# Performance work log

Measured on AMD Instinct MI355X. Metric: run time of the kernel, lower is better.

The kernel has to match this reference:

```python
import jax, jax.numpy as jnp
import numpy as np

N = 50000       # nodes
E = 600000      # edges (before self-loops)
D_IN, D_H, D_OUT, D_E = 128, 128, 64, 8
NEG_SLOPE = 0.2


def _glorot(key, shape):
    fan = shape[0]
    return jax.random.normal(key, shape, dtype=jnp.float32) / jnp.sqrt(jnp.float32(fan))


def setup_inputs() -> dict:
    key = jax.random.key(0)
    ks = iter(jax.random.split(key, 32))
    inp = {
        "x": jax.random.normal(next(ks), (N, D_IN), dtype=jnp.float32),
        "edge_index": jax.random.randint(next(ks), (2, E), 0, N, dtype=jnp.int64),
        "edge_attr": jax.random.normal(next(ks), (E, D_E), dtype=jnp.float32),
    }
    dims = [(D_IN, D_H), (D_H, D_H), (D_H, D_OUT)]  # 3 GATConv layers, heads=1
    for i, (din, dout) in enumerate(dims):
        inp[f"W{i}"] = _glorot(next(ks), (din, dout))
        inp[f"as{i}"] = _glorot(next(ks), (dout,))
        inp[f"ad{i}"] = _glorot(next(ks), (dout,))
        inp[f"We{i}"] = _glorot(next(ks), (D_E, dout))
        inp[f"ae{i}"] = _glorot(next(ks), (dout,))
        inp[f"b{i}"] = jnp.zeros((dout,), dtype=jnp.float32)
    return inp


def _add_self_loops(src, dst, edge_attr, n):
    # PyG add_self_loops(fill_value='mean'): self-loop attr = mean of incoming edge attrs
    deg = jax.ops.segment_sum(jnp.ones_like(dst, dtype=edge_attr.dtype), dst, num_segments=n)
    mean_attr = jax.ops.segment_sum(edge_attr, dst, num_segments=n) / jnp.maximum(deg, 1.0)[:, None]
    loop = jnp.arange(n, dtype=src.dtype)
    return (jnp.concatenate([src, loop]),
            jnp.concatenate([dst, loop]),
            jnp.concatenate([edge_attr, mean_attr], axis=0))


def _gat_layer(x, src, dst, edge_attr, W, a_s, a_d, We, a_e, b, n):
    h = x @ W                                   # [N, C] linear projection
    alpha = (h @ a_s)[src] + (h @ a_d)[dst] + (edge_attr @ We) @ a_e   # [Etot]
    alpha = jax.nn.leaky_relu(alpha, NEG_SLOPE)
    m = jax.ops.segment_max(alpha, dst, num_segments=n)                # segment softmax over dst
    ex = jnp.exp(alpha - m[dst])
    denom = jax.ops.segment_sum(ex, dst, num_segments=n)
    w = ex / (denom[dst] + 1e-16)
    return jax.ops.segment_sum(h[src] * w[:, None], dst, num_segments=n) + b


def reference(x, edge_index, edge_attr,
              W0, as0, ad0, We0, ae0, b0,
              W1, as1, ad1, We1, ae1, b1,
              W2, as2, ad2, We2, ae2, b2):
    n = x.shape[0]
    src, dst, ea = _add_self_loops(edge_index[0], edge_index[1], edge_attr, n)
    h = jax.nn.relu(_gat_layer(x, src, dst, ea, W0, as0, ad0, We0, ae0, b0, n))
    h = jax.nn.relu(_gat_layer(h, src, dst, ea, W1, as1, ad1, We1, ae1, b1, n))
    return _gat_layer(h, src, dst, ea, W2, as2, ad2, We2, ae2, b2, n)
```

## Files before the change

### kernel.cpp

```cpp
#include <hip/hip_runtime.h>
#include <hip/hip_fp16.h>
#include <cstdint>

#define NEG_SLOPE 0.2f
#define LOG2E 1.4426950408889634f
#define MAXD 64

typedef _Float16 f16;
typedef __attribute__((ext_vector_type(8))) _Float16 f16x8;
typedef __attribute__((ext_vector_type(4))) float f32x4;


__global__ void k_zero(int* __restrict__ p, int n) {
    int i = blockIdx.x * blockDim.x + threadIdx.x;
    if (i < n) p[i] = 0;
}

__global__ void k_wt(const float* __restrict__ W0, const float* __restrict__ W1,
                     const float* __restrict__ W2, f16* __restrict__ Wt0,
                     f16* __restrict__ Wt1, f16* __restrict__ Wt2) {
    int i = blockIdx.x * 256 + threadIdx.x;
    if (i < 16384) {
        int k = i >> 7, c = i & 127;
        Wt0[c * 128 + k] = (f16)W0[i];
    } else if (i < 32768) {
        int j = i - 16384; int k = j >> 7, c = j & 127;
        Wt1[c * 128 + k] = (f16)W1[j];
    } else if (i < 40960) {
        int j = i - 32768; int k = j >> 6, c = j & 63;
        Wt2[c * 128 + k] = (f16)W2[j];
    }
}

__global__ void k_count_fill(const int* __restrict__ src, const int* __restrict__ dst,
                             const float* __restrict__ ea,
                             const float* __restrict__ We0, const float* __restrict__ ae0,
                             const float* __restrict__ We1, const float* __restrict__ ae1,
                             const float* __restrict__ We2, const float* __restrict__ ae2,
                             int* __restrict__ deg, ushort4* __restrict__ ed, int E) {
    __shared__ float swea[24];
    int tid = threadIdx.x;
    if (tid < 24) {
        int layer = tid >> 3, k = tid & 7;
        const float* We = layer == 0 ? We0 : (layer == 1 ? We1 : We2);
        const float* ae = layer == 0 ? ae0 : (layer == 1 ? ae1 : ae2);
        int D = layer == 2 ? 64 : 128;
        float s = 0.f;
        for (int t = 0; t < D; t++) s = fmaf(We[(size_t)k * D + t], ae[t], s);
        swea[tid] = s;
    }
    __syncthreads();
    int e = blockIdx.x * blockDim.x + tid;
    if (e >= E) return;
    int s = src[e];
    int d = dst[e];
    int r = atomicAdd(deg + d, 1);
    if (r > MAXD - 1) r = MAXD - 1;
    float4 a0 = *(const float4*)&ea[(size_t)e * 8];
    float4 a1 = *(const float4*)&ea[(size_t)e * 8 + 4];
    float4 w00 = *(const float4*)&swea[0],  w01 = *(const float4*)&swea[4];
    float4 w10 = *(const float4*)&swea[8],  w11 = *(const float4*)&swea[12];
    float4 w20 = *(const float4*)&swea[16], w21 = *(const float4*)&swea[20];
    float d0 = a0.x*w00.x + a0.y*w00.y + a0.z*w00.z + a0.w*w00.w
             + a1.x*w01.x + a1.y*w01.y + a1.z*w01.z + a1.w*w01.w;
    float d1 = a0.x*w10.x + a0.y*w10.y + a0.z*w10.z + a0.w*w10.w
             + a1.x*w11.x + a1.y*w11.y + a1.z*w11.z + a1.w*w11.w;
    float d2 = a0.x*w20.x + a0.y*w20.y + a0.z*w20.z + a0.w*w20.w
             + a1.x*w21.x + a1.y*w21.y + a1.z*w21.z + a1.w*w21.w;
    ushort4 rec;
    rec.x = (unsigned short)s;
    rec.y = __half_as_ushort(__float2half(d0));
    rec.z = __half_as_ushort(__float2half(d1));
    rec.w = __half_as_ushort(__float2half(d2));
    ed[(size_t)d * MAXD + r] = rec;
}


template<int DOUT, bool XHALF>
__global__ __launch_bounds__(256) void k_gemm_mfma(
    const void* __restrict__ X_, const f16* __restrict__ Wt,
    const float* __restrict__ as_, const float* __restrict__ ad_,
    __half* __restrict__ H, float* __restrict__ hs, float* __restrict__ hd, int n)
{
    constexpr int NT = DOUT / 16;
    int lane = threadIdx.x & 63;
    int wave = threadIdx.x >> 6;
    int row0 = (blockIdx.x * 4 + wave) * 16;
    if (row0 >= n) return;
    int lrow = lane & 15;
    int kgrp = lane >> 4;
    int arow = row0 + lrow;
    bool aok = arow < n;

    f32x4 acc[NT] = {};

#pragma unroll
    for (int kt = 0; kt < 128; kt += 32) {
        f16x8 a = {};
        if (aok) {
            if constexpr (XHALF) {
                a = *(const f16x8*)((const f16*)X_ + (size_t)arow * 128 + kt + 8 * kgrp);
            } else {
                const float* xp = (const float*)X_ + (size_t)arow * 128 + kt + 8 * kgrp;
                float4 x0 = *(const float4*)xp;
                float4 x1 = *(const float4*)(xp + 4);
                f16x8 t = { (f16)x0.x, (f16)x0.y, (f16)x0.z, (f16)x0.w,
                            (f16)x1.x, (f16)x1.y, (f16)x1.z, (f16)x1.w };
                a = t;
            }
        }
#pragma unroll
        for (int nt = 0; nt < NT; nt++) {
            f16x8 b = *(const f16x8*)(Wt + (size_t)(nt * 16 + lrow) * 128 + kt + 8 * kgrp);
            acc[nt] = __builtin_amdgcn_mfma_f32_16x16x32_f16(a, b, acc[nt], 0, 0, 0);
        }
    }

    float asv[NT], adv[NT];
#pragma unroll
    for (int nt = 0; nt < NT; nt++) {
        asv[nt] = as_[nt * 16 + lrow];
        adv[nt] = ad_[nt * 16 + lrow];
    }

#pragma unroll
    for (int r = 0; r < 4; r++) {
        int row = row0 + 4 * kgrp + r;
        bool rok = row < n;
        float ps = 0.f, pd = 0.f;
#pragma unroll
        for (int nt = 0; nt < NT; nt++) {
            float v = acc[nt][r];
            ps = fmaf(v, asv[nt], ps);
            pd = fmaf(v, adv[nt], pd);
            if (rok) H[(size_t)row * DOUT + nt * 16 + lrow] = __float2half(v);
        }
#pragma unroll
        for (int off = 8; off; off >>= 1) {
            ps += __shfl_xor(ps, off);
            pd += __shfl_xor(pd, off);
        }
        if (rok && lrow == 0) { hs[row] = ps; hd[row] = pd; }
    }
}


template<int CPL>
__device__ __forceinline__ void accum_row16(float* acc, const __half* __restrict__ hrow,
                                            int l, float w) {
    if constexpr (CPL == 8) {
        float4 raw = *(const float4*)(hrow + 8 * l);
        __half2* h = (__half2*)&raw;
#pragma unroll
        for (int i = 0; i < 4; i++) {
            float2 f = __half22float2(h[i]);
            acc[2 * i]     = fmaf(w, f.x, acc[2 * i]);
            acc[2 * i + 1] = fmaf(w, f.y, acc[2 * i + 1]);
        }
    } else {
        float2 raw = *(const float2*)(hrow + 4 * l);
        __half2* h = (__half2*)&raw;
#pragma unroll
        for (int i = 0; i < 2; i++) {
            float2 f = __half22float2(h[i]);
            acc[2 * i]     = fmaf(w, f.x, acc[2 * i]);
            acc[2 * i + 1] = fmaf(w, f.y, acc[2 * i + 1]);
        }
    }
}

__device__ __forceinline__ float unpack_w(unsigned int p) {
    return __half2float(__ushort_as_half((unsigned short)(p & 0xFFFFu)));
}

__device__ __forceinline__ float fexp(float x) {
    return exp2f(x * LOG2E);
}

template<int DOUT, bool RELU, int LCOMP, bool OUT_HALF>
__global__ void k_aggregate(const __half* __restrict__ H,
                            const int* __restrict__ deg, const ushort4* __restrict__ edata,
                            const float* __restrict__ hs, const float* __restrict__ hd,
                            const float* __restrict__ bias, void* __restrict__ out_, int n) {
    int t = blockIdx.x * blockDim.x + threadIdx.x;
    int wid = t >> 6, lane = t & 63;
    if (wid >= n) return;
    int d = deg[wid]; if (d > MAXD) d = MAXD;
    int start = wid << 6;
    int quarter = lane >> 4, l = lane & 15;
    float hdv = hd[wid];
    float hsw = hs[wid];

    constexpr int CPL = DOUT / 16;
    float acc[CPL] = {};

    float al = -3.0e38f; int s = 0; float eadv = 0.f;
    if (lane < d) {
        ushort4 pv = edata[start + lane];
        s = pv.x;
        unsigned short eu = (LCOMP == 1) ? pv.y : (LCOMP == 2) ? pv.z : pv.w;
        eadv = __half2float(__ushort_as_half(eu));
        float a = hs[s] + hdv + eadv;
        al = a > 0.f ? a : NEG_SLOPE * a;
    }
    float esum = (lane < d) ? eadv : 0.f;
    float m0 = al;
#pragma unroll
    for (int off = 32; off; off >>= 1) {
        esum += __shfl_xor(esum, off);
        m0 = fmaxf(m0, __shfl_xor(m0, off));
    }
    int dd = d < 1 ? 1 : d;
    float aself = hsw + hdv + esum / (float)dd;
    aself = aself > 0.f ? aself : NEG_SLOPE * aself;
    float m = fmaxf(m0, aself);

    float ex = (lane < d) ? fexp(al - m) : 0.f;
    float exsum = ex;
#pragma unroll
    for (int off = 32; off; off >>= 1) exsum += __shfl_xor(exsum, off);
    float exself = fexp(aself - m);
    float denom = exsum + exself;

    unsigned int pk = ((unsigned int)s << 16) |
                      (unsigned int)__half_as_ushort(__float2half(ex));

    if (quarter == 0) accum_row16<CPL>(acc, H + (size_t)wid * DOUT, l, exself);

    int quads = (d + 3) >> 2;
#pragma unroll 4
    for (int jj = 0; jj < quads; jj++) {
        int j = 4 * jj + quarter;
        unsigned int pj = (unsigned int)__shfl((int)pk, j);
        int sj = pj >> 16;
        float w = unpack_w(pj);
        if (j < d) accum_row16<CPL>(acc, H + ((size_t)sj << (CPL == 8 ? 7 : 6)), l, w);
    }

#pragma unroll
    for (int v = 0; v < CPL; v++) {
        acc[v] += __shfl_xor(acc[v], 16);
        acc[v] += __shfl_xor(acc[v], 32);
    }

    if (lane < 16) {
        float inv = 1.0f / (denom + 1e-16f);
        float o[CPL];
#pragma unroll
        for (int v = 0; v < CPL; v++) {
            o[v] = acc[v] * inv + bias[CPL * l + v];
            if (RELU) o[v] = fmaxf(o[v], 0.f);
        }
        if constexpr (OUT_HALF) {
            __half* outh = (__half*)out_;
            __half2 p[CPL / 2];
#pragma unroll
            for (int v = 0; v < CPL / 2; v++) p[v] = __floats2half2_rn(o[2 * v], o[2 * v + 1]);
            if constexpr (CPL == 8) {
                *(uint4*)&outh[(size_t)wid * DOUT + 8 * l] = *(uint4*)p;
            } else {
                *(uint2*)&outh[(size_t)wid * DOUT + 4 * l] = *(uint2*)p;
            }
        } else {
            float* outf = (float*)out_;
            if constexpr (CPL == 8) {
                float4 o0 = { o[0], o[1], o[2], o[3] };
                float4 o1 = { o[4], o[5], o[6], o[7] };
                *(float4*)&outf[(size_t)wid * DOUT + 8 * l] = o0;
                *(float4*)&outf[(size_t)wid * DOUT + 8 * l + 4] = o1;
            } else {
                float4 ov = { o[0], o[1], o[2], o[3] };
                *(float4*)&outf[(size_t)wid * DOUT + 4 * l] = ov;
            }
        }
    }
}


extern "C" void kernel_launch(void* const* d_in, const int* in_sizes, int n_in,
                              void* d_out, int out_size, void* d_ws, size_t ws_size,
                              hipStream_t stream) {
    const float* x     = (const float*)d_in[0];
    const int*   eidx  = (const int*)d_in[1];
    const float* eattr = (const float*)d_in[2];
    const int N = in_sizes[0] / 128;
    const int E = in_sizes[1] / 2;
    const int* src = eidx;
    const int* dst = eidx + E;

    char* ws = (char*)d_ws;
    size_t off = 0;
    auto alloc = [&](size_t bytes) -> void* {
        void* p = ws + off;
        off += (bytes + 255) & ~(size_t)255;
        return p;
    };
    __half*  bufA = (__half*)alloc((size_t)N * 128 * sizeof(__half));
    __half*  hbuf = (__half*)alloc((size_t)N * 128 * sizeof(__half));
    int*     deg  = (int*)alloc((size_t)N * sizeof(int));
    float*   hs   = (float*)alloc((size_t)N * sizeof(float));
    float*   hd   = (float*)alloc((size_t)N * sizeof(float));
    ushort4* ed   = (ushort4*)alloc((size_t)N * MAXD * sizeof(ushort4));
    f16*     Wt0  = (f16*)alloc(16384 * sizeof(f16));
    f16*     Wt1  = (f16*)alloc(16384 * sizeof(f16));
    f16*     Wt2  = (f16*)alloc(8192 * sizeof(f16));

    const int tb = 256;

    k_zero<<<(N + tb - 1) / tb, tb, 0, stream>>>(deg, N);
    k_wt<<<160, 256, 0, stream>>>((const float*)d_in[3], (const float*)d_in[9],
                                  (const float*)d_in[15], Wt0, Wt1, Wt2);
    k_count_fill<<<(E + tb - 1) / tb, tb, 0, stream>>>(
        src, dst, eattr,
        (const float*)d_in[6], (const float*)d_in[7],
        (const float*)d_in[12], (const float*)d_in[13],
        (const float*)d_in[18], (const float*)d_in[19],
        deg, ed, E);

    int nwave_blocks = (N * 64 + tb - 1) / tb;
    int gemm_blocks = (N + 63) / 64;

    {
        const float* as_ = (const float*)d_in[4];
        const float* ad_ = (const float*)d_in[5];
        const float* b   = (const float*)d_in[8];
        k_gemm_mfma<128, false><<<gemm_blocks, 256, 0, stream>>>(x, Wt0, as_, ad_, hbuf, hs, hd, N);
        k_aggregate<128, true, 1, true><<<nwave_blocks, tb, 0, stream>>>(hbuf, deg, ed, hs, hd, b, bufA, N);
    }
    {
        const float* as_ = (const float*)d_in[10];
        const float* ad_ = (const float*)d_in[11];
        const float* b   = (const float*)d_in[14];
        k_gemm_mfma<128, true><<<gemm_blocks, 256, 0, stream>>>(bufA, Wt1, as_, ad_, hbuf, hs, hd, N);
        k_aggregate<128, true, 2, true><<<nwave_blocks, tb, 0, stream>>>(hbuf, deg, ed, hs, hd, b, bufA, N);
    }
    {
        const float* as_ = (const float*)d_in[16];
        const float* ad_ = (const float*)d_in[17];
        const float* b   = (const float*)d_in[20];
        k_gemm_mfma<64, true><<<gemm_blocks, 256, 0, stream>>>(bufA, Wt2, as_, ad_, hbuf, hs, hd, N);
        k_aggregate<64, false, 3, false><<<nwave_blocks, tb, 0, stream>>>(hbuf, deg, ed, hs, hd, b, d_out, N);
    }
}
```

Measured before the change: 226.8 us.

## Split edge count/fill, co-schedule fill with layer-0 GEMM, two nodes per wave

Edge degree counting moves into its own kernel that records per-edge rank, and the edge-attention precompute moves into the weight-transpose kernel. The edge fill then runs in the same launch as the layer-0 GEMM, with blocks interleaved so the two independent workloads overlap. Aggregation now handles two destination nodes per wave (32 lanes each), with a looped fallback for nodes of degree above 32, so fewer lanes sit idle at the average degree of about 12. This adds an extra kernel launch and a rank array round-trip through memory, and half-wave processing serialises more gather iterations per node.

```diff
diff --git a/kernel.cpp b/kernel.cpp
--- a/kernel.cpp
+++ b/kernel.cpp
@@ -16,9 +16,22 @@
     if (i < n) p[i] = 0;
 }
 
+__global__ void k_count(const int* __restrict__ dst, int* __restrict__ deg,
+                        unsigned short* __restrict__ rank, int E) {
+    int e = blockIdx.x * blockDim.x + threadIdx.x;
+    if (e < E) {
+        int r = atomicAdd(deg + dst[e], 1);
+        rank[e] = (unsigned short)(r > MAXD - 1 ? MAXD - 1 : r);
+    }
+}
+
 __global__ void k_wt(const float* __restrict__ W0, const float* __restrict__ W1,
                      const float* __restrict__ W2, f16* __restrict__ Wt0,
-                     f16* __restrict__ Wt1, f16* __restrict__ Wt2) {
+                     f16* __restrict__ Wt1, f16* __restrict__ Wt2,
+                     const float* __restrict__ We0, const float* __restrict__ ae0,
+                     const float* __restrict__ We1, const float* __restrict__ ae1,
+                     const float* __restrict__ We2, const float* __restrict__ ae2,
+                     float* __restrict__ wea) {
     int i = blockIdx.x * 256 + threadIdx.x;
     if (i < 16384) {
         int k = i >> 7, c = i & 127;
@@ -29,38 +42,34 @@
     } else if (i < 40960) {
         int j = i - 32768; int k = j >> 6, c = j & 63;
         Wt2[c * 128 + k] = (f16)W2[j];
-    }
-}
-
-__global__ void k_count_fill(const int* __restrict__ src, const int* __restrict__ dst,
-                             const float* __restrict__ ea,
-                             const float* __restrict__ We0, const float* __restrict__ ae0,
-                             const float* __restrict__ We1, const float* __restrict__ ae1,
-                             const float* __restrict__ We2, const float* __restrict__ ae2,
-                             int* __restrict__ deg, ushort4* __restrict__ ed, int E) {
-    __shared__ float swea[24];
-    int tid = threadIdx.x;
-    if (tid < 24) {
-        int layer = tid >> 3, k = tid & 7;
+    } else if (i < 40984) {
+        int j = i - 40960;
+        int layer = j >> 3, k = j & 7;
         const float* We = layer == 0 ? We0 : (layer == 1 ? We1 : We2);
         const float* ae = layer == 0 ? ae0 : (layer == 1 ? ae1 : ae2);
         int D = layer == 2 ? 64 : 128;
         float s = 0.f;
         for (int t = 0; t < D; t++) s = fmaf(We[(size_t)k * D + t], ae[t], s);
-        swea[tid] = s;
-    }
-    __syncthreads();
-    int e = blockIdx.x * blockDim.x + tid;
+        wea[j] = s;
+    }
+}
+
+
+__device__ __forceinline__ void fill_body(
+    int bid, int tid,
+    const int* __restrict__ src, const int* __restrict__ dst,
+    const unsigned short* __restrict__ rank, const float* __restrict__ ea,
+    const float* __restrict__ wea, ushort4* __restrict__ ed, int E)
+{
+    int e = bid * 256 + tid;
     if (e >= E) return;
     int s = src[e];
-    int d = dst[e];
-    int r = atomicAdd(deg + d, 1);
-    if (r > MAXD - 1) r = MAXD - 1;
+    int pos = dst[e] * MAXD + (int)rank[e];
     float4 a0 = *(const float4*)&ea[(size_t)e * 8];
     float4 a1 = *(const float4*)&ea[(size_t)e * 8 + 4];
-    float4 w00 = *(const float4*)&swea[0],  w01 = *(const float4*)&swea[4];
-    float4 w10 = *(const float4*)&swea[8],  w11 = *(const float4*)&swea[12];
-    float4 w20 = *(const float4*)&swea[16], w21 = *(const float4*)&swea[20];
+    float4 w00 = *(const float4*)&wea[0],  w01 = *(const float4*)&wea[4];
+    float4 w10 = *(const float4*)&wea[8],  w11 = *(const float4*)&wea[12];
+    float4 w20 = *(const float4*)&wea[16], w21 = *(const float4*)&wea[20];
     float d0 = a0.x*w00.x + a0.y*w00.y + a0.z*w00.z + a0.w*w00.w
              + a1.x*w01.x + a1.y*w01.y + a1.z*w01.z + a1.w*w01.w;
     float d1 = a0.x*w10.x + a0.y*w10.y + a0.z*w10.z + a0.w*w10.w
@@ -72,20 +81,20 @@
     rec.y = __half_as_ushort(__float2half(d0));
     rec.z = __half_as_ushort(__float2half(d1));
     rec.w = __half_as_ushort(__float2half(d2));
-    ed[(size_t)d * MAXD + r] = rec;
-}
-
+    ed[pos] = rec;
+}
 
 template<int DOUT, bool XHALF>
-__global__ __launch_bounds__(256) void k_gemm_mfma(
+__device__ __forceinline__ void gemm_mfma_body(
+    int bid, int tid,
     const void* __restrict__ X_, const f16* __restrict__ Wt,
     const float* __restrict__ as_, const float* __restrict__ ad_,
     __half* __restrict__ H, float* __restrict__ hs, float* __restrict__ hd, int n)
 {
     constexpr int NT = DOUT / 16;
-    int lane = threadIdx.x & 63;
-    int wave = threadIdx.x >> 6;
-    int row0 = (blockIdx.x * 4 + wave) * 16;
+    int lane = tid & 63;
+    int wave = tid >> 6;
+    int row0 = (bid * 4 + wave) * 16;
     if (row0 >= n) return;
     int lrow = lane & 15;
     int kgrp = lane >> 4;
@@ -144,6 +153,35 @@
     }
 }
 
+template<int DOUT, bool XHALF>
+__global__ __launch_bounds__(256) void k_gemm_mfma(
+    const void* __restrict__ X_, const f16* __restrict__ Wt,
+    const float* __restrict__ as_, const float* __restrict__ ad_,
+    __half* __restrict__ H, float* __restrict__ hs, float* __restrict__ hd, int n)
+{
+    gemm_mfma_body<DOUT, XHALF>(blockIdx.x, threadIdx.x, X_, Wt, as_, ad_, H, hs, hd, n);
+}
+
+__global__ __launch_bounds__(256) void k_fill_gemm0(
+    const int* __restrict__ src, const int* __restrict__ dst,
+    const unsigned short* __restrict__ rank, const float* __restrict__ ea,
+    const float* __restrict__ wea, ushort4* __restrict__ ed, int E,
+    const float* __restrict__ X, const f16* __restrict__ Wt0,
+    const float* __restrict__ as_, const float* __restrict__ ad_,
+    __half* __restrict__ H, float* __restrict__ hs, float* __restrict__ hd, int n,
+    int gemmBlocks, int totalBlocks)
+{
+    int bid = blockIdx.x, tid = threadIdx.x;
+    long long g = gemmBlocks, T = totalBlocks;
+    int before = (int)((long long)bid * g / T);
+    int after  = (int)(((long long)bid + 1) * g / T);
+    if (after > before) {
+        gemm_mfma_body<128, false>(before, tid, X, Wt0, as_, ad_, H, hs, hd, n);
+    } else {
+        fill_body(bid - before, tid, src, dst, rank, ea, wea, ed, E);
+    }
+}
+
 
 template<int CPL>
 __device__ __forceinline__ void accum_row16(float* acc, const __half* __restrict__ hrow,
@@ -177,73 +215,129 @@
     return exp2f(x * LOG2E);
 }
 
+__device__ __forceinline__ float leaky(float a) {
+    return a > 0.f ? a : NEG_SLOPE * a;
+}
+
 template<int DOUT, bool RELU, int LCOMP, bool OUT_HALF>
 __global__ void k_aggregate(const __half* __restrict__ H,
                             const int* __restrict__ deg, const ushort4* __restrict__ edata,
                             const float* __restrict__ hs, const float* __restrict__ hd,
                             const float* __restrict__ bias, void* __restrict__ out_, int n) {
     int t = blockIdx.x * blockDim.x + threadIdx.x;
-    int wid = t >> 6, lane = t & 63;
-    if (wid >= n) return;
-    int d = deg[wid]; if (d > MAXD) d = MAXD;
-    int start = wid << 6;
-    int quarter = lane >> 4, l = lane & 15;
-    float hdv = hd[wid];
-    float hsw = hs[wid];
+    int w = t >> 6, lane = t & 63;
+    if (2 * w >= n) return;
+    int half = lane >> 5, ln = lane & 31;
+    int node = 2 * w + half;
+    bool active = node < n;
+    int d = active ? deg[node] : 0; if (d > MAXD) d = MAXD;
+    int start = node << 6;
+    float hdv = active ? hd[node] : 0.f;
+    float hsw = active ? hs[node] : 0.f;
+    int q = ln >> 4, l = ln & 15;
 
     constexpr int CPL = DOUT / 16;
     float acc[CPL] = {};
-
-    float al = -3.0e38f; int s = 0; float eadv = 0.f;
-    if (lane < d) {
-        ushort4 pv = edata[start + lane];
-        s = pv.x;
-        unsigned short eu = (LCOMP == 1) ? pv.y : (LCOMP == 2) ? pv.z : pv.w;
-        eadv = __half2float(__ushort_as_half(eu));
-        float a = hs[s] + hdv + eadv;
-        al = a > 0.f ? a : NEG_SLOPE * a;
-    }
-    float esum = (lane < d) ? eadv : 0.f;
-    float m0 = al;
-#pragma unroll
-    for (int off = 32; off; off >>= 1) {
-        esum += __shfl_xor(esum, off);
-        m0 = fmaxf(m0, __shfl_xor(m0, off));
-    }
-    int dd = d < 1 ? 1 : d;
-    float aself = hsw + hdv + esum / (float)dd;
-    aself = aself > 0.f ? aself : NEG_SLOPE * aself;
-    float m = fmaxf(m0, aself);
-
-    float ex = (lane < d) ? fexp(al - m) : 0.f;
-    float exsum = ex;
-#pragma unroll
-    for (int off = 32; off; off >>= 1) exsum += __shfl_xor(exsum, off);
-    float exself = fexp(aself - m);
-    float denom = exsum + exself;
-
-    unsigned int pk = ((unsigned int)s << 16) |
-                      (unsigned int)__half_as_ushort(__float2half(ex));
-
-    if (quarter == 0) accum_row16<CPL>(acc, H + (size_t)wid * DOUT, l, exself);
-
-    int quads = (d + 3) >> 2;
-#pragma unroll 4
-    for (int jj = 0; jj < quads; jj++) {
-        int j = 4 * jj + quarter;
-        unsigned int pj = (unsigned int)__shfl((int)pk, j);
-        int sj = pj >> 16;
-        float w = unpack_w(pj);
-        if (j < d) accum_row16<CPL>(acc, H + ((size_t)sj << (CPL == 8 ? 7 : 6)), l, w);
-    }
-
-#pragma unroll
-    for (int v = 0; v < CPL; v++) {
-        acc[v] += __shfl_xor(acc[v], 16);
-        acc[v] += __shfl_xor(acc[v], 32);
-    }
-
-    if (lane < 16) {
+    float denom;
+
+    int dmx = d;
+    dmx = max(dmx, __shfl_xor(dmx, 32));
+
+    if (dmx <= 32) {
+        float al = -3.0e38f; int s = 0; float eadv = 0.f;
+        if (ln < d) {
+            ushort4 pv = edata[start + ln];
+            s = pv.x;
+            unsigned short eu = (LCOMP == 1) ? pv.y : (LCOMP == 2) ? pv.z : pv.w;
+            eadv = __half2float(__ushort_as_half(eu));
+            al = leaky(hs[s] + hdv + eadv);
+        }
+        float esum = (ln < d) ? eadv : 0.f;
+        float m0 = al;
+#pragma unroll
+        for (int off = 16; off; off >>= 1) {
+            esum += __shfl_xor(esum, off);
+            m0 = fmaxf(m0, __shfl_xor(m0, off));
+        }
+        int dd = d < 1 ? 1 : d;
+        float aself = leaky(hsw + hdv + esum / (float)dd);
+        float m = fmaxf(m0, aself);
+
+        float ex = (ln < d) ? fexp(al - m) : 0.f;
+        float exsum = ex;
+#pragma unroll
+        for (int off = 16; off; off >>= 1) exsum += __shfl_xor(exsum, off);
+        float exself = fexp(aself - m);
+        denom = exsum + exself;
+
+        unsigned int pk = ((unsigned int)s << 16) |
+                          (unsigned int)__half_as_ushort(__float2half(ex));
+
+        if (active && q == 0) accum_row16<CPL>(acc, H + (size_t)node * DOUT, l, exself);
+
+        int pairs = (d + 1) >> 1;
+        for (int jj = 0; jj < pairs; jj++) {
+            int j = 2 * jj + q;
+            unsigned int pj = (unsigned int)__shfl((int)pk, half * 32 + j);
+            int sj = pj >> 16;
+            float wt = unpack_w(pj);
+            if (j < d) accum_row16<CPL>(acc, H + (size_t)sj * DOUT, l, wt);
+        }
+    } else {
+        float esum = 0.f, m0 = -3.0e38f;
+        for (int base = 0; base < d; base += 32) {
+            if (base + ln < d) {
+                ushort4 pv = edata[start + base + ln];
+                unsigned short eu = (LCOMP == 1) ? pv.y : (LCOMP == 2) ? pv.z : pv.w;
+                float ev = __half2float(__ushort_as_half(eu));
+                esum += ev;
+                m0 = fmaxf(m0, leaky(hs[pv.x] + hdv + ev));
+            }
+        }
+#pragma unroll
+        for (int off = 16; off; off >>= 1) {
+            esum += __shfl_xor(esum, off);
+            m0 = fmaxf(m0, __shfl_xor(m0, off));
+        }
+        int dd = d < 1 ? 1 : d;
+        float aself = leaky(hsw + hdv + esum / (float)dd);
+        float m = fmaxf(m0, aself);
+        float exself = fexp(aself - m);
+        denom = exself;
+        if (active && q == 0) accum_row16<CPL>(acc, H + (size_t)node * DOUT, l, exself);
+
+        int dw = dmx;
+        for (int base = 0; base < dw; base += 32) {
+            float ex = 0.f; int s = 0;
+            if (base + ln < d) {
+                ushort4 pv = edata[start + base + ln];
+                s = pv.x;
+                unsigned short eu = (LCOMP == 1) ? pv.y : (LCOMP == 2) ? pv.z : pv.w;
+                ex = fexp(leaky(hs[s] + hdv + __half2float(__ushort_as_half(eu))) - m);
+            }
+            float exsum = ex;
+#pragma unroll
+            for (int off = 16; off; off >>= 1) exsum += __shfl_xor(exsum, off);
+            denom += exsum;
+            unsigned int pk = ((unsigned int)s << 16) |
+                              (unsigned int)__half_as_ushort(__float2half(ex));
+            int rem = d - base; if (rem > 32) rem = 32; if (rem < 0) rem = 0;
+            int pairs = (rem + 1) >> 1;
+            int pmax = pairs; pmax = max(pmax, __shfl_xor(pmax, 32));
+            for (int jj = 0; jj < pmax; jj++) {
+                int j = 2 * jj + q;
+                unsigned int pj = (unsigned int)__shfl((int)pk, half * 32 + j);
+                int sj = pj >> 16;
+                float wt = unpack_w(pj);
+                if (j < rem) accum_row16<CPL>(acc, H + (size_t)sj * DOUT, l, wt);
+            }
+        }
+    }
+
+#pragma unroll
+    for (int v = 0; v < CPL; v++) acc[v] += __shfl_xor(acc[v], 16);
+
+    if (active && q == 0) {
         float inv = 1.0f / (denom + 1e-16f);
         float o[CPL];
 #pragma unroll
@@ -257,20 +351,20 @@
 #pragma unroll
             for (int v = 0; v < CPL / 2; v++) p[v] = __floats2half2_rn(o[2 * v], o[2 * v + 1]);
             if constexpr (CPL == 8) {
-                *(uint4*)&outh[(size_t)wid * DOUT + 8 * l] = *(uint4*)p;
+                *(uint4*)&outh[(size_t)node * DOUT + 8 * l] = *(uint4*)p;
             } else {
-                *(uint2*)&outh[(size_t)wid * DOUT + 4 * l] = *(uint2*)p;
+                *(uint2*)&outh[(size_t)node * DOUT + 4 * l] = *(uint2*)p;
             }
         } else {
             float* outf = (float*)out_;
             if constexpr (CPL == 8) {
                 float4 o0 = { o[0], o[1], o[2], o[3] };
                 float4 o1 = { o[4], o[5], o[6], o[7] };
-                *(float4*)&outf[(size_t)wid * DOUT + 8 * l] = o0;
-                *(float4*)&outf[(size_t)wid * DOUT + 8 * l + 4] = o1;
+                *(float4*)&outf[(size_t)node * DOUT + 8 * l] = o0;
+                *(float4*)&outf[(size_t)node * DOUT + 8 * l + 4] = o1;
             } else {
                 float4 ov = { o[0], o[1], o[2], o[3] };
-                *(float4*)&outf[(size_t)wid * DOUT + 4 * l] = ov;
+                *(float4*)&outf[(size_t)node * DOUT + 4 * l] = ov;
             }
         }
     }
@@ -295,50 +389,55 @@
         off += (bytes + 255) & ~(size_t)255;
         return p;
     };
-    __half*  bufA = (__half*)alloc((size_t)N * 128 * sizeof(__half));
-    __half*  hbuf = (__half*)alloc((size_t)N * 128 * sizeof(__half));
-    int*     deg  = (int*)alloc((size_t)N * sizeof(int));
-    float*   hs   = (float*)alloc((size_t)N * sizeof(float));
-    float*   hd   = (float*)alloc((size_t)N * sizeof(float));
-    ushort4* ed   = (ushort4*)alloc((size_t)N * MAXD * sizeof(ushort4));
-    f16*     Wt0  = (f16*)alloc(16384 * sizeof(f16));
-    f16*     Wt1  = (f16*)alloc(16384 * sizeof(f16));
-    f16*     Wt2  = (f16*)alloc(8192 * sizeof(f16));
+    __half*         bufA = (__half*)alloc((size_t)N * 128 * sizeof(__half));
+    __half*         hbuf = (__half*)alloc((size_t)N * 128 * sizeof(__half));
+    int*            deg  = (int*)alloc((size_t)N * sizeof(int));
+    float*          hs   = (float*)alloc((size_t)N * sizeof(float));
+    float*          hd   = (float*)alloc((size_t)N * sizeof(float));
+    ushort4*        ed   = (ushort4*)alloc((size_t)N * MAXD * sizeof(ushort4));
+    unsigned short* rank = (unsigned short*)alloc((size_t)E * sizeof(unsigned short));
+    f16*            Wt0  = (f16*)alloc(16384 * sizeof(f16));
+    f16*            Wt1  = (f16*)alloc(16384 * sizeof(f16));
+    f16*            Wt2  = (f16*)alloc(8192 * sizeof(f16));
+    float*          wea  = (float*)alloc(64 * sizeof(float));
 
     const int tb = 256;
 
     k_zero<<<(N + tb - 1) / tb, tb, 0, stream>>>(deg, N);
-    k_wt<<<160, 256, 0, stream>>>((const float*)d_in[3], (const float*)d_in[9],
-                                  (const float*)d_in[15], Wt0, Wt1, Wt2);
-    k_count_fill<<<(E + tb - 1) / tb, tb, 0, stream>>>(
-        src, dst, eattr,
-        (const float*)d_in[6], (const float*)d_in[7],
-        (const float*)d_in[12], (const float*)d_in[13],
-        (const float*)d_in[18], (const float*)d_in[19],
-        deg, ed, E);
-
-    int nwave_blocks = (N * 64 + tb - 1) / tb;
+    k_count<<<(E + tb - 1) / tb, tb, 0, stream>>>(dst, deg, rank, E);
+    k_wt<<<161, 256, 0, stream>>>((const float*)d_in[3], (const float*)d_in[9],
+                                  (const float*)d_in[15], Wt0, Wt1, Wt2,
+                                  (const float*)d_in[6], (const float*)d_in[7],
+                                  (const float*)d_in[12], (const float*)d_in[13],
+                                  (const float*)d_in[18], (const float*)d_in[19], wea);
+
+    int agg_blocks = (N + 7) / 8;
     int gemm_blocks = (N + 63) / 64;
 
     {
         const float* as_ = (const float*)d_in[4];
         const float* ad_ = (const float*)d_in[5];
-        const float* b   = (const float*)d_in[8];
-        k_gemm_mfma<128, false><<<gemm_blocks, 256, 0, stream>>>(x, Wt0, as_, ad_, hbuf, hs, hd, N);
-        k_aggregate<128, true, 1, true><<<nwave_blocks, tb, 0, stream>>>(hbuf, deg, ed, hs, hd, b, bufA, N);
+        int fillBlocks = (E + tb - 1) / tb;
+        int totalBlocks = fillBlocks + gemm_blocks;
+        k_fill_gemm0<<<totalBlocks, tb, 0, stream>>>(
+            src, dst, rank, eattr, wea, ed, E,
+            x, Wt0, as_, ad_, hbuf, hs, hd, N,
+            gemm_blocks, totalBlocks);
+        const float* b = (const float*)d_in[8];
+        k_aggregate<128, true, 1, true><<<agg_blocks, tb, 0, stream>>>(hbuf, deg, ed, hs, hd, b, bufA, N);
     }
     {
         const float* as_ = (const float*)d_in[10];
         const float* ad_ = (const float*)d_in[11];
         const float* b   = (const float*)d_in[14];
         k_gemm_mfma<128, true><<<gemm_blocks, 256, 0, stream>>>(bufA, Wt1, as_, ad_, hbuf, hs, hd, N);
-        k_aggregate<128, true, 2, true><<<nwave_blocks, tb, 0, stream>>>(hbuf, deg, ed, hs, hd, b, bufA, N);
+        k_aggregate<128, true, 2, true><<<agg_blocks, tb, 0, stream>>>(hbuf, deg, ed, hs, hd, b, bufA, N);
     }
     {
         const float* as_ = (const float*)d_in[16];
         const float* ad_ = (const float*)d_in[17];
         const float* b   = (const float*)d_in[20];
         k_gemm_mfma<64, true><<<gemm_blocks, 256, 0, stream>>>(bufA, Wt2, as_, ad_, hbuf, hs, hd, N);
-        k_aggregate<64, false, 3, false><<<nwave_blocks, tb, 0, stream>>>(hbuf, deg, ed, hs, hd, b, d_out, N);
-    }
-}
+        k_aggregate<64, false, 3, false><<<agg_blocks, tb, 0, stream>>>(hbuf, deg, ed, hs, hd, b, d_out, N);
+    }
+}
```

After: 217.2 us. 1.04x faster.
